# Kernel optimization log

Measured on AMD Instinct MI355X. Metric: run time of the kernel, lower is better.

Reference implementation:

```python
import jax, jax.numpy as jnp
import numpy as np

GAMMA = 10.0

def setup_inputs() -> dict:
    key = jax.random.key(0)
    B, N, D = 9, 4096, 2048
    # scale so gamma * squared pairwise distances is O(1) (mimics normalized features)
    x = jax.random.normal(key, (B, N, D), dtype=jnp.float32) * 0.01
    return {"x": x}

def reference(x):
    # x: [B, N, D]; pairwise per-sample squared distances via the GEMM identity
    # ||a-b||^2 = ||a||^2 + ||b||^2 - 2<a,b>
    B = x.shape[0]
    s = jnp.sum(x * x, axis=-1)                      # [B, N]
    dots = jnp.einsum('ind,jnd->ijn', x, x)          # [B, B, N]
    sq = jnp.maximum(s[:, None, :] + s[None, :, :] - 2.0 * dots, 0.0)  # [B, B, N]
    snm = jnp.mean(jnp.exp(-GAMMA * sq), axis=-1)    # [B, B]
    snm = jnp.where(jnp.eye(B, dtype=bool), 0.0, snm)  # i != j only
    direct_div = jnp.sum(snm)
    det_div = -jnp.linalg.det(snm)
    sign, logabs = jnp.linalg.slogdet(snm)
    # torch.logdet returns NaN for non-positive determinant
    logdet_div = -jnp.where(sign > 0, logabs, jnp.nan)
    return (direct_div, det_div, logdet_div)
```

## Files before the change

### kernel.cpp

```cpp
#include <hip/hip_runtime.h>
#include <math.h>

#define BB 9
#define NN 4096
#define DD 2048
#define NPAIR 45
#define NOFF 36
#define WSCOL 64

__global__ void zero_ws_kernel(float* __restrict__ ws) {
    int t = blockIdx.x * blockDim.x + threadIdx.x;
    if (t < NOFF * WSCOL) ws[t] = 0.0f;
}

__global__ __launch_bounds__(256, 4) void pairdot_kernel(const float* __restrict__ x,
                                                         float* __restrict__ ws) {
    const int wave = threadIdx.x >> 6;
    const int lane = threadIdx.x & 63;
    const int n = blockIdx.x * 4 + wave;

    float acc[NPAIR];
#pragma unroll
    for (int p = 0; p < NPAIR; ++p) acc[p] = 0.0f;

    const size_t rowstride = (size_t)NN * DD;
    const float* base = x + (size_t)n * DD + (size_t)(lane * 4);

#pragma unroll 2
    for (int c = 0; c < 8; ++c) {
        float4 v[BB];
#pragma unroll
        for (int i = 0; i < BB; ++i) {
            v[i] = *(const float4*)(base + (size_t)i * rowstride + c * 256);
        }
        int p = 0;
#pragma unroll
        for (int i = 0; i < BB; ++i) {
#pragma unroll
            for (int j = i; j < BB; ++j) {
                acc[p] += v[i].x * v[j].x + v[i].y * v[j].y
                        + v[i].z * v[j].z + v[i].w * v[j].w;
                ++p;
            }
        }
    }

#pragma unroll
    for (int p = 0; p < NPAIR; ++p) {
        float a = acc[p];
#pragma unroll
        for (int m = 32; m >= 1; m >>= 1) a += __shfl_xor(a, m, 64);
        acc[p] = a;
    }

    __shared__ float sums[4][NOFF];
    if (lane == 0) {
        int q = 0;
        int p = 0;
#pragma unroll
        for (int i = 0; i < BB; ++i) {
            const int di = i * BB - i * (i - 1) / 2;
            ++p;
#pragma unroll
            for (int j = i + 1; j < BB; ++j) {
                const int dj = j * BB - j * (j - 1) / 2;
                float sq = acc[di] + acc[dj] - 2.0f * acc[p];
                sq = fmaxf(sq, 0.0f);
                sums[wave][q] = __expf(-10.0f * sq);
                ++q; ++p;
            }
        }
    }
    __syncthreads();
    if (threadIdx.x < NOFF) {
        float t = sums[0][threadIdx.x] + sums[1][threadIdx.x]
                + sums[2][threadIdx.x] + sums[3][threadIdx.x];
        atomicAdd(&ws[threadIdx.x * WSCOL + (blockIdx.x & (WSCOL - 1))], t);
    }
}

__global__ void finalize_kernel(const float* __restrict__ ws, float* __restrict__ out) {
    if (threadIdx.x != 0 || blockIdx.x != 0) return;

    double snm[BB][BB];
    for (int i = 0; i < BB; ++i)
        for (int j = 0; j < BB; ++j) snm[i][j] = 0.0;

    int q = 0;
    for (int i = 0; i < BB; ++i) {
        for (int j = i + 1; j < BB; ++j, ++q) {
            double s = 0.0;
            for (int k = 0; k < WSCOL; ++k) s += (double)ws[q * WSCOL + k];
            s /= (double)NN;
            snm[i][j] = s;
            snm[j][i] = s;
        }
    }

    double direct = 0.0;
    for (int i = 0; i < BB; ++i)
        for (int j = 0; j < BB; ++j) direct += snm[i][j];

    double M[BB][BB];
    for (int i = 0; i < BB; ++i)
        for (int j = 0; j < BB; ++j) M[i][j] = snm[i][j];

    double det = 1.0;
    for (int k = 0; k < BB; ++k) {
        int piv = k;
        double mx = fabs(M[k][k]);
        for (int r = k + 1; r < BB; ++r) {
            double a = fabs(M[r][k]);
            if (a > mx) { mx = a; piv = r; }
        }
        if (piv != k) {
            for (int c = 0; c < BB; ++c) {
                double t = M[k][c]; M[k][c] = M[piv][c]; M[piv][c] = t;
            }
            det = -det;
        }
        double pk = M[k][k];
        det *= pk;
        if (pk != 0.0) {
            for (int r = k + 1; r < BB; ++r) {
                double f = M[r][k] / pk;
                for (int c = k; c < BB; ++c) M[r][c] -= f * M[k][c];
            }
        }
    }

    out[0] = (float)direct;
    out[1] = (float)(-det);
    out[2] = (det > 0.0) ? (float)(-log(det)) : __builtin_nanf("");
}

extern "C" void kernel_launch(void* const* d_in, const int* in_sizes, int n_in,
                              void* d_out, int out_size, void* d_ws, size_t ws_size,
                              hipStream_t stream) {
    const float* x = (const float*)d_in[0];
    float* out = (float*)d_out;
    float* ws = (float*)d_ws;

    zero_ws_kernel<<<(NOFF * WSCOL + 255) / 256, 256, 0, stream>>>(ws);
    pairdot_kernel<<<NN / 4, 256, 0, stream>>>(x, ws);
    finalize_kernel<<<1, 64, 0, stream>>>(ws, out);
}
```

Baseline: 494.5 us.

## Fuse finalize into main kernel via last-block counter and parallel LU

Replaces the atomicAdd into a 64-column workspace with per-block partial stores. A global completion counter lets the last block do the reduction and determinant, so the separate finalize launch goes away. The reduction is spread over four waves and the 9x9 LU elimination runs across threads in shared memory instead of a single serial thread. It also changes the main loop unroll from 2 to 1, and it adds fences and a tail of syncthreads-heavy work in one block.

```diff
diff --git a/kernel.cpp b/kernel.cpp
--- a/kernel.cpp
+++ b/kernel.cpp
@@ -6,17 +6,20 @@
 #define DD 2048
 #define NPAIR 45
 #define NOFF 36
-#define WSCOL 64
+#define NBLK 1024
 
-__global__ void zero_ws_kernel(float* __restrict__ ws) {
-    int t = blockIdx.x * blockDim.x + threadIdx.x;
-    if (t < NOFF * WSCOL) ws[t] = 0.0f;
+
+__global__ void init_kernel(unsigned int* __restrict__ counter) {
+    if (threadIdx.x == 0 && blockIdx.x == 0) *counter = 0u;
 }
 
-__global__ __launch_bounds__(256, 4) void pairdot_kernel(const float* __restrict__ x,
-                                                         float* __restrict__ ws) {
-    const int wave = threadIdx.x >> 6;
-    const int lane = threadIdx.x & 63;
+__global__ __launch_bounds__(256, 4) void fused_kernel(const float* __restrict__ x,
+                                                       float* __restrict__ partials,
+                                                       unsigned int* __restrict__ counter,
+                                                       float* __restrict__ out) {
+    const int tid = threadIdx.x;
+    const int wave = tid >> 6;
+    const int lane = tid & 63;
     const int n = blockIdx.x * 4 + wave;
 
     float acc[NPAIR];
@@ -26,7 +29,7 @@
     const size_t rowstride = (size_t)NN * DD;
     const float* base = x + (size_t)n * DD + (size_t)(lane * 4);
 
-#pragma unroll 2
+#pragma unroll 1
     for (int c = 0; c < 8; ++c) {
         float4 v[BB];
 #pragma unroll
@@ -72,66 +75,102 @@
         }
     }
     __syncthreads();
-    if (threadIdx.x < NOFF) {
-        float t = sums[0][threadIdx.x] + sums[1][threadIdx.x]
-                + sums[2][threadIdx.x] + sums[3][threadIdx.x];
-        atomicAdd(&ws[threadIdx.x * WSCOL + (blockIdx.x & (WSCOL - 1))], t);
+    if (tid < NOFF) {
+        float t = sums[0][tid] + sums[1][tid] + sums[2][tid] + sums[3][tid];
+        __hip_atomic_store(&partials[tid * NBLK + blockIdx.x], t,
+                           __ATOMIC_RELAXED, __HIP_MEMORY_SCOPE_AGENT);
     }
-}
+    __threadfence();
+    __syncthreads();
 
-__global__ void finalize_kernel(const float* __restrict__ ws, float* __restrict__ out) {
-    if (threadIdx.x != 0 || blockIdx.x != 0) return;
+    __shared__ int lastflag;
+    if (tid == 0) {
+        unsigned int old = __hip_atomic_fetch_add(counter, 1u,
+                                                  __ATOMIC_ACQ_REL,
+                                                  __HIP_MEMORY_SCOPE_AGENT);
+        lastflag = (old == NBLK - 1) ? 1 : 0;
+    }
+    __syncthreads();
+    if (!lastflag) return;
 
-    double snm[BB][BB];
-    for (int i = 0; i < BB; ++i)
-        for (int j = 0; j < BB; ++j) snm[i][j] = 0.0;
+    __threadfence();
 
-    int q = 0;
-    for (int i = 0; i < BB; ++i) {
-        for (int j = i + 1; j < BB; ++j, ++q) {
-            double s = 0.0;
-            for (int k = 0; k < WSCOL; ++k) s += (double)ws[q * WSCOL + k];
-            s /= (double)NN;
-            snm[i][j] = s;
-            snm[j][i] = s;
+    __shared__ float snm_f[NOFF];
+#pragma unroll 1
+    for (int t = 0; t < 9; ++t) {
+        const int q = wave * 9 + t;
+        float s = 0.0f;
+#pragma unroll
+        for (int k = 0; k < NBLK / 64; ++k) {
+            s += __hip_atomic_load(&partials[q * NBLK + k * 64 + lane],
+                                   __ATOMIC_RELAXED, __HIP_MEMORY_SCOPE_AGENT);
+        }
+#pragma unroll
+        for (int m = 32; m >= 1; m >>= 1) s += __shfl_xor(s, m, 64);
+        if (lane == 0) snm_f[q] = s;
+    }
+    __syncthreads();
+
+    __shared__ double A[BB * BB];
+    __shared__ double Fs[BB];
+    __shared__ int piv_s;
+
+    const double inv_n = 1.0 / (double)NN;
+    if (tid < BB * BB) {
+        const int r = tid / BB, c = tid % BB;
+        if (r == c) {
+            A[tid] = 0.0;
+        } else {
+            const int i = r < c ? r : c;
+            const int j = r < c ? c : r;
+            const int q = i * (2 * BB - 1 - i) / 2 + (j - i - 1);
+            A[tid] = (double)snm_f[q] * inv_n;
         }
     }
+    __syncthreads();
 
-    double direct = 0.0;
-    for (int i = 0; i < BB; ++i)
-        for (int j = 0; j < BB; ++j) direct += snm[i][j];
-
-    double M[BB][BB];
-    for (int i = 0; i < BB; ++i)
-        for (int j = 0; j < BB; ++j) M[i][j] = snm[i][j];
-
-    double det = 1.0;
-    for (int k = 0; k < BB; ++k) {
-        int piv = k;
-        double mx = fabs(M[k][k]);
-        for (int r = k + 1; r < BB; ++r) {
-            double a = fabs(M[r][k]);
-            if (a > mx) { mx = a; piv = r; }
-        }
-        if (piv != k) {
-            for (int c = 0; c < BB; ++c) {
-                double t = M[k][c]; M[k][c] = M[piv][c]; M[piv][c] = t;
-            }
-            det = -det;
-        }
-        double pk = M[k][k];
-        det *= pk;
-        if (pk != 0.0) {
-            for (int r = k + 1; r < BB; ++r) {
-                double f = M[r][k] / pk;
-                for (int c = k; c < BB; ++c) M[r][c] -= f * M[k][c];
-            }
-        }
+    double direct = 0.0, detv = 1.0;
+    if (tid == 0) {
+        for (int q = 0; q < NOFF; ++q) direct += (double)snm_f[q];
+        direct = 2.0 * direct * inv_n;
     }
 
-    out[0] = (float)direct;
-    out[1] = (float)(-det);
-    out[2] = (det > 0.0) ? (float)(-log(det)) : __builtin_nanf("");
+    for (int k = 0; k < BB; ++k) {
+        if (tid == 0) {
+            int piv = k;
+            double mx = fabs(A[k * BB + k]);
+            for (int r = k + 1; r < BB; ++r) {
+                double a = fabs(A[r * BB + k]);
+                if (a > mx) { mx = a; piv = r; }
+            }
+            piv_s = piv;
+        }
+        __syncthreads();
+        const int piv = piv_s;
+        double tk = 0.0, tp = 0.0;
+        if (tid < BB) { tk = A[k * BB + tid]; tp = A[piv * BB + tid]; }
+        __syncthreads();
+        if (tid < BB) { A[k * BB + tid] = tp; A[piv * BB + tid] = tk; }
+        __syncthreads();
+        if (tid == 0) {
+            detv *= A[k * BB + k];
+            if (piv != k) detv = -detv;
+        }
+        if (tid > k && tid < BB) Fs[tid] = A[tid * BB + k] / A[k * BB + k];
+        __syncthreads();
+        if (tid < BB * BB) {
+            const int r = tid / BB, c = tid % BB;
+            if (r > k && c >= k) A[tid] -= Fs[r] * A[k * BB + c];
+        }
+        __syncthreads();
+    }
+
+    if (tid == 0) {
+        out[0] = (float)direct;
+        out[1] = (float)(-detv);
+        out[2] = (detv > 0.0) ? (float)(-log(detv))
+                              : __builtin_nanf("");
+    }
 }
 
 extern "C" void kernel_launch(void* const* d_in, const int* in_sizes, int n_in,
@@ -139,9 +178,9 @@
                               hipStream_t stream) {
     const float* x = (const float*)d_in[0];
     float* out = (float*)d_out;
-    float* ws = (float*)d_ws;
+    float* partials = (float*)d_ws;
+    unsigned int* counter = (unsigned int*)d_ws + NOFF * NBLK;
 
-    zero_ws_kernel<<<(NOFF * WSCOL + 255) / 256, 256, 0, stream>>>(ws);
-    pairdot_kernel<<<NN / 4, 256, 0, stream>>>(x, ws);
-    finalize_kernel<<<1, 64, 0, stream>>>(ws, out);
+    init_kernel<<<1, 64, 0, stream>>>(counter);
+    fused_kernel<<<NBLK, 256, 0, stream>>>(x, partials, counter, out);
 }
```

New measurement: 483.2 us. 1.02x faster.
